# Kernel tuning notes

Hardware: AMD Instinct MI355X
Metric: run time of the kernel (lower is better)

The kernel has to match this reference:

```python
import jax, jax.numpy as jnp
import numpy as np

N = 100000      # nodes
E = 1600000     # edges (before self-loops)
IN_DIM = 128
HID = 32
HEADS = 4
EMB = 128
SLOPE = 0.2     # PyG GATConv default negative_slope


def setup_inputs() -> dict:
    key = jax.random.key(0)
    ks = jax.random.split(key, 16)
    def glorot(k, shape):
        fan_in = shape[0] if len(shape) > 1 else shape[-1]
        return jax.random.normal(k, shape, jnp.float32) * (1.0 / np.sqrt(fan_in))
    x = jax.random.normal(ks[0], (N, IN_DIM), jnp.float32)
    edge_index = jax.random.randint(ks[1], (2, E), 0, N)
    return {
        "x": x,
        "edge_index": edge_index,
        # layer 1: in_dim -> hidden (heads=4, concat)
        "W1": glorot(ks[2], (IN_DIM, HEADS * HID)),
        "att_src1": glorot(ks[3], (HEADS, HID)),
        "att_dst1": glorot(ks[4], (HEADS, HID)),
        "b1": jnp.zeros((HEADS * HID,), jnp.float32),
        # layer 2: hidden*heads -> hidden (heads=4, concat)
        "W2": glorot(ks[5], (HEADS * HID, HEADS * HID)),
        "att_src2": glorot(ks[6], (HEADS, HID)),
        "att_dst2": glorot(ks[7], (HEADS, HID)),
        "b2": jnp.zeros((HEADS * HID,), jnp.float32),
        # layer 3: hidden*heads -> embed (heads=1)
        "W3": glorot(ks[8], (HEADS * HID, EMB)),
        "att_src3": glorot(ks[9], (1, EMB)),
        "att_dst3": glorot(ks[10], (1, EMB)),
        "b3": jnp.zeros((EMB,), jnp.float32),
    }


def gat_conv(x, src, dst, W, att_src, att_dst, b, heads, out_ch):
    """One PyG-style GATConv (concat=True). src/dst already include self-loops."""
    n = x.shape[0]
    h = (x @ W).reshape(n, heads, out_ch)                 # [N,H,C]
    a_s = jnp.einsum('nhc,hc->nh', h, att_src)            # [N,H]
    a_d = jnp.einsum('nhc,hc->nh', h, att_dst)            # [N,H]
    e = jax.nn.leaky_relu(a_s[src] + a_d[dst], SLOPE)     # [E',H]
    # numerically stable softmax over irregular incoming neighborhoods (per dst)
    m = jax.ops.segment_max(e, dst, num_segments=n)       # [N,H]
    ex = jnp.exp(e - m[dst])
    denom = jax.ops.segment_sum(ex, dst, num_segments=n)  # [N,H]
    alpha = ex / denom[dst]                                # [E',H]
    out = jax.ops.segment_sum(h[src] * alpha[:, :, None], dst, num_segments=n)
    return out.reshape(n, heads * out_ch) + b


def reference(x, edge_index, W1, att_src1, att_dst1, b1,
              W2, att_src2, att_dst2, b2, W3, att_src3, att_dst3, b3):
    n = x.shape[0]
    loops = jnp.arange(n, dtype=edge_index.dtype)
    src = jnp.concatenate([edge_index[0], loops])  # PyG add_self_loops=True
    dst = jnp.concatenate([edge_index[1], loops])
    h = gat_conv(x, src, dst, W1, att_src1, att_dst1, b1, HEADS, HID)
    h = jax.nn.elu(h)
    h = gat_conv(h, src, dst, W2, att_src2, att_dst2, b2, HEADS, HID)
    h = jax.nn.elu(h)
    out = gat_conv(h, src, dst, W3, att_src3, att_dst3, b3, 1, EMB)
    return out
```

## Files before the change

kernel.cpp:

```cpp
#include <hip/hip_runtime.h>
#include <hip/hip_fp16.h>
#include <math.h>

#define N_NODES 100000
#define N_EDGES 1600000
#define SLOPE 0.2f

#define BSHIFT 8
#define NB 391
#define CHUNK 8192

typedef _Float16 f16x8 __attribute__((ext_vector_type(8)));
typedef float f32x4 __attribute__((ext_vector_type(4)));

__global__ __launch_bounds__(256) void partA1(const int* __restrict__ ei,
                                              int* __restrict__ bucket_count,
                                              int E, int n) {
  __shared__ int cnt[NB];
  for (int i = threadIdx.x; i < NB; i += 256) cnt[i] = 0;
  __syncthreads();
  int base = blockIdx.x * CHUNK;
  int total = E + n;
  int lim = min(base + CHUNK, total);
  for (int e = base + threadIdx.x; e < lim; e += 256) {
    int d = (e < E) ? ei[E + e] : (e - E);
    atomicAdd(&cnt[d >> BSHIFT], 1);
  }
  __syncthreads();
  for (int i = threadIdx.x; i < NB; i += 256)
    if (cnt[i]) atomicAdd(&bucket_count[i], cnt[i]);
}

__global__ __launch_bounds__(512) void scan_nb(
    const int* __restrict__ bucket_count, int* __restrict__ bucket_base,
    int* __restrict__ bucket_cursor) {
  __shared__ int lds[512];
  int t = threadIdx.x;
  int v = (t < NB) ? bucket_count[t] : 0;
  int x = v;
  lds[t] = x;
  __syncthreads();
  for (int off = 1; off < 512; off <<= 1) {
    int y = (t >= off) ? lds[t - off] : 0;
    __syncthreads();
    x += y;
    lds[t] = x;
    __syncthreads();
  }
  int excl = x - v;
  if (t <= NB) bucket_base[t] = excl;
  if (t < NB) bucket_cursor[t] = excl;
}

__global__ __launch_bounds__(256) void partA2(const int* __restrict__ ei,
                                              int* __restrict__ bucket_cursor,
                                              unsigned* __restrict__ part,
                                              int E, int n) {
  __shared__ int cnt[NB];
  __shared__ int res[NB];
  for (int i = threadIdx.x; i < NB; i += 256) cnt[i] = 0;
  __syncthreads();
  int base = blockIdx.x * CHUNK;
  int total = E + n;
  int lim = min(base + CHUNK, total);
  for (int e = base + threadIdx.x; e < lim; e += 256) {
    int d = (e < E) ? ei[E + e] : (e - E);
    atomicAdd(&cnt[d >> BSHIFT], 1);
  }
  __syncthreads();
  for (int i = threadIdx.x; i < NB; i += 256)
    res[i] = cnt[i] ? atomicAdd(&bucket_cursor[i], cnt[i]) : 0;
  __syncthreads();
  for (int e = base + threadIdx.x; e < lim; e += 256) {
    int s, d;
    if (e < E) { s = ei[e]; d = ei[E + e]; } else { s = d = e - E; }
    int b = d >> BSHIFT;
    int pos = atomicAdd(&res[b], 1);
    part[pos] = ((unsigned)s << BSHIFT) | (unsigned)(d & 255);
  }
}

__global__ __launch_bounds__(256) void passB(const unsigned* __restrict__ part,
                                             const int* __restrict__ bucket_base,
                                             int* __restrict__ row_start,
                                             int* __restrict__ edge_src, int n) {
  __shared__ int cnt[256];
  __shared__ int sc[256];
  __shared__ int loff[256];
  int b = blockIdx.x;
  int t = threadIdx.x;
  int node0 = b << BSHIFT;
  int bstart = bucket_base[b], bend = bucket_base[b + 1];
  cnt[t] = 0;
  __syncthreads();
  for (int i = bstart + t; i < bend; i += 256)
    atomicAdd(&cnt[part[i] & 255], 1);
  __syncthreads();
  int v = cnt[t];
  int x = v;
  sc[t] = x;
  __syncthreads();
  for (int off = 1; off < 256; off <<= 1) {
    int y = (t >= off) ? sc[t - off] : 0;
    __syncthreads();
    x += y;
    sc[t] = x;
    __syncthreads();
  }
  int excl = x - v;
  loff[t] = excl;
  int node = node0 + t;
  if (node < n) row_start[node] = bstart + excl;
  if (b == NB - 1 && t == 0) row_start[n] = bucket_base[NB];
  __syncthreads();
  for (int i = bstart + t; i < bend; i += 256) {
    unsigned p = part[i];
    int dl = p & 255;
    int pos = bstart + atomicAdd(&loff[dl], 1);
    edge_src[pos] = (int)(p >> BSHIFT);
  }
}

__global__ __launch_bounds__(256) void convert_w(
    const float* __restrict__ W1, const float* __restrict__ W2,
    const float* __restrict__ W3, __half* __restrict__ Wt1,
    __half* __restrict__ Wt2, __half* __restrict__ Wt3) {
  int idx = blockIdx.x * 256 + threadIdx.x;
  if (idx >= 3 * 16384) return;
  int mat = idx >> 14;
  int r = idx & 16383;
  int k = r >> 7, col = r & 127;
  const float* W = (mat == 0) ? W1 : (mat == 1) ? W2 : W3;
  __half* Wt = (mat == 0) ? Wt1 : (mat == 1) ? Wt2 : Wt3;
  Wt[col * 128 + k] = __float2half(W[k * 128 + col]);
}

template <int H>
__global__ __launch_bounds__(256) void gemm_att_mfma(
    const float* __restrict__ X, const __half* __restrict__ Wt,
    const float* __restrict__ att_src, const float* __restrict__ att_dst,
    __half* __restrict__ Y, float* __restrict__ a_s, float* __restrict__ a_d,
    int n) {
  __shared__ _Float16 A_lds[64 * 128];
  __shared__ _Float16 B_lds[128 * 128];
  int t = threadIdx.x;
  int r0 = blockIdx.x * 64;

  {
    int row = t >> 2;
    int c0 = (t & 3) * 32;
    const float* xp = X + (size_t)(r0 + row) * 128 + c0;
    bool inb = (r0 + row) < n;
#pragma unroll
    for (int i = 0; i < 8; i++) {
      float4 v;
      if (inb) v = *(const float4*)(xp + i * 4);
      else v = make_float4(0.f, 0.f, 0.f, 0.f);
      union { float2 f; __half2 h2[2]; } u;
      u.h2[0] = __floats2half2_rn(v.x, v.y);
      u.h2[1] = __floats2half2_rn(v.z, v.w);
      *(float2*)&A_lds[row * 128 + c0 + i * 4] = u.f;
    }
  }
  {
    const __half* wp = Wt + t * 64;
#pragma unroll
    for (int i = 0; i < 8; i++)
      *(float4*)&B_lds[t * 64 + i * 8] = *(const float4*)(wp + i * 8);
  }
  __syncthreads();

  int wv = t >> 6, lane = t & 63, quad = lane >> 4, l15 = lane & 15;
  const _Float16* Arow = &A_lds[(wv * 16 + l15) * 128];
  f32x4 acc[8];
#pragma unroll
  for (int ct = 0; ct < 8; ct++) acc[ct] = (f32x4){0.f, 0.f, 0.f, 0.f};

#pragma unroll
  for (int kb = 0; kb < 4; kb++) {
    f16x8 a = *(const f16x8*)(Arow + kb * 32 + quad * 8);
#pragma unroll
    for (int ct = 0; ct < 8; ct++) {
      f16x8 b = *(const f16x8*)(&B_lds[(ct * 16 + l15) * 128 + kb * 32 + quad * 8]);
      acc[ct] = __builtin_amdgcn_mfma_f32_16x16x32_f16(a, b, acc[ct], 0, 0, 0);
    }
  }

  int rbase = r0 + wv * 16 + quad * 4;
#pragma unroll
  for (int reg = 0; reg < 4; reg++) {
    int row = rbase + reg;
    if (row < n) {
#pragma unroll
      for (int ct = 0; ct < 8; ct++)
        Y[(size_t)row * 128 + ct * 16 + l15] = __float2half(acc[ct][reg]);
    }
  }

  float avs[8], avd[8];
#pragma unroll
  for (int ct = 0; ct < 8; ct++) {
    avs[ct] = att_src[ct * 16 + l15];
    avd[ct] = att_dst[ct * 16 + l15];
  }
  if constexpr (H == 4) {
    float ps[4][4], pd_[4][4];
#pragma unroll
    for (int hd = 0; hd < 4; hd++)
#pragma unroll
      for (int reg = 0; reg < 4; reg++) { ps[hd][reg] = 0.f; pd_[hd][reg] = 0.f; }
#pragma unroll
    for (int ct = 0; ct < 8; ct++) {
      int hd = ct >> 1;
#pragma unroll
      for (int reg = 0; reg < 4; reg++) {
        ps[hd][reg] = fmaf(acc[ct][reg], avs[ct], ps[hd][reg]);
        pd_[hd][reg] = fmaf(acc[ct][reg], avd[ct], pd_[hd][reg]);
      }
    }
#pragma unroll
    for (int off = 1; off <= 8; off <<= 1)
#pragma unroll
      for (int hd = 0; hd < 4; hd++)
#pragma unroll
        for (int reg = 0; reg < 4; reg++) {
          ps[hd][reg] += __shfl_xor(ps[hd][reg], off, 64);
          pd_[hd][reg] += __shfl_xor(pd_[hd][reg], off, 64);
        }
#pragma unroll
    for (int hd = 0; hd < 4; hd++)
      if (l15 == hd) {
#pragma unroll
        for (int reg = 0; reg < 4; reg++) {
          int row = rbase + reg;
          if (row < n) {
            a_s[row * 4 + hd] = ps[hd][reg];
            a_d[row * 4 + hd] = pd_[hd][reg];
          }
        }
      }
  } else {
    float ps[4] = {}, pd_[4] = {};
#pragma unroll
    for (int ct = 0; ct < 8; ct++)
#pragma unroll
      for (int reg = 0; reg < 4; reg++) {
        ps[reg] = fmaf(acc[ct][reg], avs[ct], ps[reg]);
        pd_[reg] = fmaf(acc[ct][reg], avd[ct], pd_[reg]);
      }
#pragma unroll
    for (int off = 1; off <= 8; off <<= 1)
#pragma unroll
      for (int reg = 0; reg < 4; reg++) {
        ps[reg] += __shfl_xor(ps[reg], off, 64);
        pd_[reg] += __shfl_xor(pd_[reg], off, 64);
      }
    if (l15 == 0) {
#pragma unroll
      for (int reg = 0; reg < 4; reg++) {
        int row = rbase + reg;
        if (row < n) { a_s[row] = ps[reg]; a_d[row] = pd_[reg]; }
      }
    }
  }
}

template <int H, bool DO_ELU>
__global__ __launch_bounds__(256) void agg_kernel(
    const __half* __restrict__ h, const float* __restrict__ a_s,
    const float* __restrict__ a_d, const int* __restrict__ row_start,
    const int* __restrict__ edge_src, const float* __restrict__ bias,
    float* __restrict__ out, int n) {
  const int C = 128 / H;
  __shared__ float w_lds[4][H * 66];
  __shared__ int sn_lds[4][64];
  int wslot = threadIdx.x >> 6;
  int wid = (blockIdx.x * blockDim.x + threadIdx.x) >> 6;
  int lane = threadIdx.x & 63;
  if (wid >= n) return;
  int start = row_start[wid], end = row_start[wid + 1];
  int deg = end - start;

  float adv[H];
#pragma unroll
  for (int hh = 0; hh < H; hh++) adv[hh] = a_d[wid * H + hh];

  if (deg <= 64) {
    bool valid = lane < deg;
    int sn = valid ? edge_src[start + lane] : 0;
    float e[H];
    if (valid) {
      if constexpr (H == 4) {
        float4 asv = *(const float4*)(a_s + (size_t)sn * 4);
        float t0 = asv.x + adv[0];
        float t1 = asv.y + adv[1];
        float t2 = asv.z + adv[2];
        float t3 = asv.w + adv[3];
        e[0] = t0 >= 0.f ? t0 : SLOPE * t0;
        e[1] = t1 >= 0.f ? t1 : SLOPE * t1;
        e[2] = t2 >= 0.f ? t2 : SLOPE * t2;
        e[3] = t3 >= 0.f ? t3 : SLOPE * t3;
      } else {
        float tt = a_s[sn] + adv[0];
        e[0] = tt >= 0.f ? tt : SLOPE * tt;
      }
    } else {
#pragma unroll
      for (int hh = 0; hh < H; hh++) e[hh] = -1e30f;
    }
    bool small = (deg <= 32);
    float w[H], s[H];
#pragma unroll
    for (int hh = 0; hh < H; hh++) {
      w[hh] = valid ? __expf(e[hh] - 40.f) : 0.f;
      s[hh] = w[hh];
    }
#pragma unroll
    for (int off = 1; off <= 16; off <<= 1)
#pragma unroll
      for (int hh = 0; hh < H; hh++) s[hh] += __shfl_xor(s[hh], off, 64);
    if (!small)
#pragma unroll
      for (int hh = 0; hh < H; hh++) s[hh] += __shfl_xor(s[hh], 32, 64);
    sn_lds[wslot][lane] = sn << 8;
#pragma unroll
    for (int hh = 0; hh < H; hh++)
      w_lds[wslot][hh * 66 + lane] = valid ? w[hh] * (1.f / s[hh]) : 0.f;
    __builtin_amdgcn_wave_barrier();

    int g = lane >> 5, l = lane & 31;
    int d0 = l * 4;
    int dby = l * 8;
    int headBase = (H == 4) ? (l >> 3) * 66 : 0;
    float acc0 = 0.f, acc1 = 0.f, acc2 = 0.f, acc3 = 0.f;
    int degp4 = (deg + 3) & ~3;
    for (int eidx = g; eidx < degp4; eidx += 4) {
#pragma unroll
      for (int jj = 0; jj < 2; jj++) {
        int ei2 = eidx + jj * 2;
        int boff = sn_lds[wslot][ei2] + dby;
        float wv = w_lds[wslot][headBase + ei2];
        union { float2 f; __half2 h2[2]; } u;
        u.f = *(const float2*)((const char*)h + (unsigned)boff);
        float2 p0 = __half22float2(u.h2[0]);
        float2 p1 = __half22float2(u.h2[1]);
        acc0 = fmaf(p0.x, wv, acc0);
        acc1 = fmaf(p0.y, wv, acc1);
        acc2 = fmaf(p1.x, wv, acc2);
        acc3 = fmaf(p1.y, wv, acc3);
      }
    }
    acc0 += __shfl_xor(acc0, 32, 64);
    acc1 += __shfl_xor(acc1, 32, 64);
    acc2 += __shfl_xor(acc2, 32, 64);
    acc3 += __shfl_xor(acc3, 32, 64);
    if (lane < 32) {
      float4 bv = *(const float4*)(bias + d0);
      float o0 = acc0 + bv.x, o1 = acc1 + bv.y;
      float o2 = acc2 + bv.z, o3 = acc3 + bv.w;
      if (DO_ELU) {
        o0 = (o0 > 0.f) ? o0 : __expf(o0) - 1.f;
        o1 = (o1 > 0.f) ? o1 : __expf(o1) - 1.f;
        o2 = (o2 > 0.f) ? o2 : __expf(o2) - 1.f;
        o3 = (o3 > 0.f) ? o3 : __expf(o3) - 1.f;
      }
      float4 ov = {o0, o1, o2, o3};
      *(float4*)(out + (size_t)wid * 128 + d0) = ov;
    }
    return;
  }

  {
    const int G = C / 2;
    int head = lane / G;
    float m[H], s[H];
#pragma unroll
    for (int hh = 0; hh < H; hh++) { m[hh] = -1e30f; s[hh] = 0.f; }
    for (int idx = start + lane; idx < end; idx += 64) {
      int sn = edge_src[idx];
#pragma unroll
      for (int hh = 0; hh < H; hh++) {
        float e = a_s[sn * H + hh] + adv[hh];
        e = (e >= 0.f) ? e : SLOPE * e;
        float mn = fmaxf(m[hh], e);
        s[hh] = s[hh] * __expf(m[hh] - mn) + __expf(e - mn);
        m[hh] = mn;
      }
    }
    for (int off = 1; off < 64; off <<= 1) {
#pragma unroll
      for (int hh = 0; hh < H; hh++) {
        float mo = __shfl_xor(m[hh], off, 64);
        float so = __shfl_xor(s[hh], off, 64);
        float mn = fmaxf(m[hh], mo);
        s[hh] = s[hh] * __expf(m[hh] - mn) + so * __expf(mo - mn);
        m[hh] = mn;
      }
    }
    int d0 = lane * 2;
    float mh = m[head];
    float rsh = 1.f / s[head];
    float adh = adv[head];
    float acc0 = 0.f, acc1 = 0.f;
    for (int idx = start; idx < end; idx++) {
      int sn = edge_src[idx];
      float e = a_s[sn * H + head] + adh;
      e = (e >= 0.f) ? e : SLOPE * e;
      float w = __expf(e - mh) * rsh;
      float2 hv = __half22float2(*(const __half2*)(h + (size_t)sn * 128 + d0));
      acc0 += w * hv.x;
      acc1 += w * hv.y;
    }
    float o0 = acc0 + bias[d0];
    float o1 = acc1 + bias[d0 + 1];
    if (DO_ELU) {
      o0 = (o0 > 0.f) ? o0 : __expf(o0) - 1.f;
      o1 = (o1 > 0.f) ? o1 : __expf(o1) - 1.f;
    }
    out[(size_t)wid * 128 + d0] = o0;
    out[(size_t)wid * 128 + d0 + 1] = o1;
  }
}

extern "C" void kernel_launch(void* const* d_in, const int* in_sizes, int n_in,
                              void* d_out, int out_size, void* d_ws,
                              size_t ws_size, hipStream_t stream) {
  const float* x = (const float*)d_in[0];
  const int* ei = (const int*)d_in[1];
  const float* W1 = (const float*)d_in[2];
  const float* as1 = (const float*)d_in[3];
  const float* ad1 = (const float*)d_in[4];
  const float* b1 = (const float*)d_in[5];
  const float* W2 = (const float*)d_in[6];
  const float* as2 = (const float*)d_in[7];
  const float* ad2 = (const float*)d_in[8];
  const float* b2 = (const float*)d_in[9];
  const float* W3 = (const float*)d_in[10];
  const float* as3 = (const float*)d_in[11];
  const float* ad3 = (const float*)d_in[12];
  const float* b3 = (const float*)d_in[13];
  float* out = (float*)d_out;

  const int n = N_NODES, E = N_EDGES, total = E + n;

  char* ws = (char*)d_ws;
  size_t off = 0;
  auto alloc = [&](size_t bytes) -> char* {
    char* p = ws + off;
    off = (off + bytes + 255) & ~(size_t)255;
    return p;
  };
  __half* hbuf = (__half*)alloc(sizeof(__half) * (size_t)n * 128);
  float* a_s = (float*)alloc(sizeof(float) * n * 4);
  float* a_d = (float*)alloc(sizeof(float) * n * 4);
  unsigned* part = (unsigned*)alloc(sizeof(unsigned) * total);
  int* edge_src = (int*)alloc(sizeof(int) * total);
  int* row_start = (int*)alloc(sizeof(int) * (n + 1));
  int* bucket_count = (int*)alloc(sizeof(int) * (NB + 1));
  int* bucket_base = (int*)alloc(sizeof(int) * (NB + 1));
  int* bucket_cursor = (int*)alloc(sizeof(int) * (NB + 1));
  __half* Wt1 = (__half*)alloc(sizeof(__half) * 16384);
  __half* Wt2 = (__half*)alloc(sizeof(__half) * 16384);
  __half* Wt3 = (__half*)alloc(sizeof(__half) * 16384);

  hipMemsetAsync(bucket_count, 0, sizeof(int) * (NB + 1), stream);

  convert_w<<<192, 256, 0, stream>>>(W1, W2, W3, Wt1, Wt2, Wt3);

  int nblkA = (total + CHUNK - 1) / CHUNK;
  partA1<<<nblkA, 256, 0, stream>>>(ei, bucket_count, E, n);
  scan_nb<<<1, 512, 0, stream>>>(bucket_count, bucket_base, bucket_cursor);
  partA2<<<nblkA, 256, 0, stream>>>(ei, bucket_cursor, part, E, n);
  passB<<<NB, 256, 0, stream>>>(part, bucket_base, row_start, edge_src, n);

  int agg_blocks = (n + 3) / 4;
  int gemm_blocks = (n + 63) / 64;

  gemm_att_mfma<4><<<gemm_blocks, 256, 0, stream>>>(x, Wt1, as1, ad1, hbuf,
                                                    a_s, a_d, n);
  agg_kernel<4, true><<<agg_blocks, 256, 0, stream>>>(
      hbuf, a_s, a_d, row_start, edge_src, b1, out, n);

  gemm_att_mfma<4><<<gemm_blocks, 256, 0, stream>>>(out, Wt2, as2, ad2, hbuf,
                                                    a_s, a_d, n);
  agg_kernel<4, true><<<agg_blocks, 256, 0, stream>>>(
      hbuf, a_s, a_d, row_start, edge_src, b2, out, n);

  gemm_att_mfma<1><<<gemm_blocks, 256, 0, stream>>>(out, Wt3, as3, ad3, hbuf,
                                                    a_s, a_d, n);
  agg_kernel<1, false><<<agg_blocks, 256, 0, stream>>>(
      hbuf, a_s, a_d, row_start, edge_src, b3, out, n);
}
```

Baseline: 519.8 us.

## Store intermediate layer activations in fp16 and widen aggregation gathers to 16 bytes

Layers 1 and 2 now write their post-ELU activations as fp16 into a separate workspace buffer, and the next layer's GEMM reads fp16 directly, skipping the fp32-to-fp16 conversion. This halves the activation write and read traffic between layers, but it only applies when the workspace is large enough. The aggregation fast path also changes lane mapping: each lane gathers 8 halves (16 bytes) per neighbor, four edge groups run in parallel, and a two-step shuffle reduction combines them. This cuts instruction count per gathered byte, while adding accumulator registers and extra padding work for low-degree nodes.

```diff
diff --git a/kernel.cpp b/kernel.cpp
--- a/kernel.cpp
+++ b/kernel.cpp
@@ -135,9 +135,9 @@
   Wt[col * 128 + k] = __float2half(W[k * 128 + col]);
 }
 
-template <int H>
+template <int H, typename InT>
 __global__ __launch_bounds__(256) void gemm_att_mfma(
-    const float* __restrict__ X, const __half* __restrict__ Wt,
+    const InT* __restrict__ X, const __half* __restrict__ Wt,
     const float* __restrict__ att_src, const float* __restrict__ att_dst,
     __half* __restrict__ Y, float* __restrict__ a_s, float* __restrict__ a_d,
     int n) {
@@ -149,17 +149,28 @@
   {
     int row = t >> 2;
     int c0 = (t & 3) * 32;
-    const float* xp = X + (size_t)(r0 + row) * 128 + c0;
     bool inb = (r0 + row) < n;
-#pragma unroll
-    for (int i = 0; i < 8; i++) {
-      float4 v;
-      if (inb) v = *(const float4*)(xp + i * 4);
-      else v = make_float4(0.f, 0.f, 0.f, 0.f);
-      union { float2 f; __half2 h2[2]; } u;
-      u.h2[0] = __floats2half2_rn(v.x, v.y);
-      u.h2[1] = __floats2half2_rn(v.z, v.w);
-      *(float2*)&A_lds[row * 128 + c0 + i * 4] = u.f;
+    if constexpr (sizeof(InT) == 4) {
+      const float* xp = (const float*)X + (size_t)(r0 + row) * 128 + c0;
+#pragma unroll
+      for (int i = 0; i < 8; i++) {
+        float4 v;
+        if (inb) v = *(const float4*)(xp + i * 4);
+        else v = make_float4(0.f, 0.f, 0.f, 0.f);
+        union { float2 f; __half2 h2[2]; } u;
+        u.h2[0] = __floats2half2_rn(v.x, v.y);
+        u.h2[1] = __floats2half2_rn(v.z, v.w);
+        *(float2*)&A_lds[row * 128 + c0 + i * 4] = u.f;
+      }
+    } else {
+      const __half* xp = (const __half*)X + (size_t)(r0 + row) * 128 + c0;
+#pragma unroll
+      for (int i = 0; i < 4; i++) {
+        float4 v;
+        if (inb) v = *(const float4*)(xp + i * 8);
+        else v = make_float4(0.f, 0.f, 0.f, 0.f);
+        *(float4*)&A_lds[row * 128 + c0 + i * 8] = v;
+      }
     }
   }
   {
@@ -265,12 +276,12 @@
   }
 }
 
-template <int H, bool DO_ELU>
+template <int H, bool DO_ELU, typename OutT>
 __global__ __launch_bounds__(256) void agg_kernel(
     const __half* __restrict__ h, const float* __restrict__ a_s,
     const float* __restrict__ a_d, const int* __restrict__ row_start,
     const int* __restrict__ edge_src, const float* __restrict__ bias,
-    float* __restrict__ out, int n) {
+    OutT* __restrict__ out, int n) {
   const int C = 128 / H;
   __shared__ float w_lds[4][H * 66];
   __shared__ int sn_lds[4][64];
@@ -328,44 +339,67 @@
       w_lds[wslot][hh * 66 + lane] = valid ? w[hh] * (1.f / s[hh]) : 0.f;
     __builtin_amdgcn_wave_barrier();
 
-    int g = lane >> 5, l = lane & 31;
-    int d0 = l * 4;
-    int dby = l * 8;
-    int headBase = (H == 4) ? (l >> 3) * 66 : 0;
-    float acc0 = 0.f, acc1 = 0.f, acc2 = 0.f, acc3 = 0.f;
-    int degp4 = (deg + 3) & ~3;
-    for (int eidx = g; eidx < degp4; eidx += 4) {
-#pragma unroll
-      for (int jj = 0; jj < 2; jj++) {
-        int ei2 = eidx + jj * 2;
+    int g = lane >> 4, l = lane & 15;
+    int d0 = l * 8;
+    int dby = l * 16;
+    int headBase = (H == 4) ? (l >> 2) * 66 : 0;
+    float acc[8];
+#pragma unroll
+    for (int k = 0; k < 8; k++) acc[k] = 0.f;
+    int degp16 = (deg + 15) & ~15;
+    for (int eidx = 0; eidx < degp16; eidx += 16) {
+#pragma unroll
+      for (int jj = 0; jj < 4; jj++) {
+        int ei2 = eidx + jj * 4 + g;
         int boff = sn_lds[wslot][ei2] + dby;
         float wv = w_lds[wslot][headBase + ei2];
-        union { float2 f; __half2 h2[2]; } u;
-        u.f = *(const float2*)((const char*)h + (unsigned)boff);
+        union { float4 f; __half2 h2[4]; } u;
+        u.f = *(const float4*)((const char*)h + (unsigned)boff);
         float2 p0 = __half22float2(u.h2[0]);
         float2 p1 = __half22float2(u.h2[1]);
-        acc0 = fmaf(p0.x, wv, acc0);
-        acc1 = fmaf(p0.y, wv, acc1);
-        acc2 = fmaf(p1.x, wv, acc2);
-        acc3 = fmaf(p1.y, wv, acc3);
-      }
-    }
-    acc0 += __shfl_xor(acc0, 32, 64);
-    acc1 += __shfl_xor(acc1, 32, 64);
-    acc2 += __shfl_xor(acc2, 32, 64);
-    acc3 += __shfl_xor(acc3, 32, 64);
-    if (lane < 32) {
-      float4 bv = *(const float4*)(bias + d0);
-      float o0 = acc0 + bv.x, o1 = acc1 + bv.y;
-      float o2 = acc2 + bv.z, o3 = acc3 + bv.w;
+        float2 p2 = __half22float2(u.h2[2]);
+        float2 p3 = __half22float2(u.h2[3]);
+        acc[0] = fmaf(p0.x, wv, acc[0]);
+        acc[1] = fmaf(p0.y, wv, acc[1]);
+        acc[2] = fmaf(p1.x, wv, acc[2]);
+        acc[3] = fmaf(p1.y, wv, acc[3]);
+        acc[4] = fmaf(p2.x, wv, acc[4]);
+        acc[5] = fmaf(p2.y, wv, acc[5]);
+        acc[6] = fmaf(p3.x, wv, acc[6]);
+        acc[7] = fmaf(p3.y, wv, acc[7]);
+      }
+    }
+#pragma unroll
+    for (int k = 0; k < 8; k++) {
+      acc[k] += __shfl_xor(acc[k], 16, 64);
+      acc[k] += __shfl_xor(acc[k], 32, 64);
+    }
+    if (lane < 16) {
+      float4 bv0 = *(const float4*)(bias + d0);
+      float4 bv1 = *(const float4*)(bias + d0 + 4);
+      float o[8];
+      o[0] = acc[0] + bv0.x; o[1] = acc[1] + bv0.y;
+      o[2] = acc[2] + bv0.z; o[3] = acc[3] + bv0.w;
+      o[4] = acc[4] + bv1.x; o[5] = acc[5] + bv1.y;
+      o[6] = acc[6] + bv1.z; o[7] = acc[7] + bv1.w;
       if (DO_ELU) {
-        o0 = (o0 > 0.f) ? o0 : __expf(o0) - 1.f;
-        o1 = (o1 > 0.f) ? o1 : __expf(o1) - 1.f;
-        o2 = (o2 > 0.f) ? o2 : __expf(o2) - 1.f;
-        o3 = (o3 > 0.f) ? o3 : __expf(o3) - 1.f;
-      }
-      float4 ov = {o0, o1, o2, o3};
-      *(float4*)(out + (size_t)wid * 128 + d0) = ov;
+#pragma unroll
+        for (int k = 0; k < 8; k++)
+          o[k] = (o[k] > 0.f) ? o[k] : __expf(o[k]) - 1.f;
+      }
+      if constexpr (sizeof(OutT) == 2) {
+        union { float4 f4; __half2 h2[4]; } uo;
+        uo.h2[0] = __floats2half2_rn(o[0], o[1]);
+        uo.h2[1] = __floats2half2_rn(o[2], o[3]);
+        uo.h2[2] = __floats2half2_rn(o[4], o[5]);
+        uo.h2[3] = __floats2half2_rn(o[6], o[7]);
+        *(float4*)((__half*)out + (size_t)wid * 128 + d0) = uo.f4;
+      } else {
+        float4 ov0 = {o[0], o[1], o[2], o[3]};
+        float4 ov1 = {o[4], o[5], o[6], o[7]};
+        *(float4*)((float*)out + (size_t)wid * 128 + d0) = ov0;
+        *(float4*)((float*)out + (size_t)wid * 128 + d0 + 4) = ov1;
+      }
     }
     return;
   }
@@ -417,8 +451,8 @@
       o0 = (o0 > 0.f) ? o0 : __expf(o0) - 1.f;
       o1 = (o1 > 0.f) ? o1 : __expf(o1) - 1.f;
     }
-    out[(size_t)wid * 128 + d0] = o0;
-    out[(size_t)wid * 128 + d0 + 1] = o1;
+    out[(size_t)wid * 128 + d0] = (OutT)o0;
+    out[(size_t)wid * 128 + d0 + 1] = (OutT)o1;
   }
 }
 
@@ -462,6 +496,8 @@
   __half* Wt1 = (__half*)alloc(sizeof(__half) * 16384);
   __half* Wt2 = (__half*)alloc(sizeof(__half) * 16384);
   __half* Wt3 = (__half*)alloc(sizeof(__half) * 16384);
+  __half* hbuf2 = (__half*)alloc(sizeof(__half) * (size_t)n * 128);
+  bool fp16mid = (off <= ws_size);
 
   hipMemsetAsync(bucket_count, 0, sizeof(int) * (NB + 1), stream);
 
@@ -476,18 +512,35 @@
   int agg_blocks = (n + 3) / 4;
   int gemm_blocks = (n + 63) / 64;
 
-  gemm_att_mfma<4><<<gemm_blocks, 256, 0, stream>>>(x, Wt1, as1, ad1, hbuf,
-                                                    a_s, a_d, n);
-  agg_kernel<4, true><<<agg_blocks, 256, 0, stream>>>(
-      hbuf, a_s, a_d, row_start, edge_src, b1, out, n);
-
-  gemm_att_mfma<4><<<gemm_blocks, 256, 0, stream>>>(out, Wt2, as2, ad2, hbuf,
-                                                    a_s, a_d, n);
-  agg_kernel<4, true><<<agg_blocks, 256, 0, stream>>>(
-      hbuf, a_s, a_d, row_start, edge_src, b2, out, n);
-
-  gemm_att_mfma<1><<<gemm_blocks, 256, 0, stream>>>(out, Wt3, as3, ad3, hbuf,
-                                                    a_s, a_d, n);
-  agg_kernel<1, false><<<agg_blocks, 256, 0, stream>>>(
-      hbuf, a_s, a_d, row_start, edge_src, b3, out, n);
-}
+  if (fp16mid) {
+    gemm_att_mfma<4, float><<<gemm_blocks, 256, 0, stream>>>(
+        x, Wt1, as1, ad1, hbuf, a_s, a_d, n);
+    agg_kernel<4, true, __half><<<agg_blocks, 256, 0, stream>>>(
+        hbuf, a_s, a_d, row_start, edge_src, b1, hbuf2, n);
+
+    gemm_att_mfma<4, __half><<<gemm_blocks, 256, 0, stream>>>(
+        hbuf2, Wt2, as2, ad2, hbuf, a_s, a_d, n);
+    agg_kernel<4, true, __half><<<agg_blocks, 256, 0, stream>>>(
+        hbuf, a_s, a_d, row_start, edge_src, b2, hbuf2, n);
+
+    gemm_att_mfma<1, __half><<<gemm_blocks, 256, 0, stream>>>(
+        hbuf2, Wt3, as3, ad3, hbuf, a_s, a_d, n);
+    agg_kernel<1, false, float><<<agg_blocks, 256, 0, stream>>>(
+        hbuf, a_s, a_d, row_start, edge_src, b3, out, n);
+  } else {
+    gemm_att_mfma<4, float><<<gemm_blocks, 256, 0, stream>>>(
+        x, Wt1, as1, ad1, hbuf, a_s, a_d, n);
+    agg_kernel<4, true, float><<<agg_blocks, 256, 0, stream>>>(
+        hbuf, a_s, a_d, row_start, edge_src, b1, out, n);
+
+    gemm_att_mfma<4, float><<<gemm_blocks, 256, 0, stream>>>(
+        out, Wt2, as2, ad2, hbuf, a_s, a_d, n);
+    agg_kernel<4, true, float><<<agg_blocks, 256, 0, stream>>>(
+        hbuf, a_s, a_d, row_start, edge_src, b2, out, n);
+
+    gemm_att_mfma<1, float><<<gemm_blocks, 256, 0, stream>>>(
+        out, Wt3, as3, ad3, hbuf, a_s, a_d, n);
+    agg_kernel<1, false, float><<<agg_blocks, 256, 0, stream>>>(
+        hbuf, a_s, a_d, row_start, edge_src, b3, out, n);
+  }
+}
```

Measured after the change: 496.5 us. 1.05x faster.
